# Performance work log

Hardware: AMD Instinct MI355X
Metric: run time of the kernel (lower is better)

The kernel has to match this reference:

```python
import jax, jax.numpy as jnp
import numpy as np

# S6Layer dims: d_model=256; internal d_state=max(8,16//2)=8; expand=max(1.5,2*0.75)=1.5 -> d_inner=384
B, L, DM = 8, 4096, 256
DI, DS = 384, 8
CHUNK = 32  # seq_len > 64 path: chunked scan, state resets to 0 at every chunk (faithful to source)
EPS = 1e-5


def setup_inputs() -> dict:
    key = jax.random.key(0)
    ks = jax.random.split(key, 8)
    def w(k, shape, s=0.02):
        return jax.random.normal(k, shape, jnp.float32) * s
    return {
        "x": jax.random.normal(ks[0], (B, L, DM), jnp.float32),
        "gamma": jnp.ones((DM,), jnp.float32),
        "beta": jnp.zeros((DM,), jnp.float32),
        "W_in": w(ks[1], (3 * DI, DM)),
        "b_in": jnp.zeros((3 * DI,), jnp.float32),
        "W_dt": w(ks[2], (DI, DI)),
        "b_dt": jnp.zeros((DI,), jnp.float32),
        "A_log": jax.random.normal(ks[3], (DI, DS), jnp.float32),
        "D_vec": jax.random.normal(ks[4], (DI,), jnp.float32),
        "W_out": w(ks[5], (DM, DI)),
        "b_out": jnp.zeros((DM,), jnp.float32),
    }


def _layernorm(x, g, b):
    mu = jnp.mean(x, axis=-1, keepdims=True)
    var = jnp.mean(jnp.square(x - mu), axis=-1, keepdims=True)
    return (x - mu) * jax.lax.rsqrt(var + EPS) * g + b


def _chunked_scan(xp, dt, A):
    # xp, dt: [B, L, DI]; A: [DI, DS]. Each CHUNK-length block scans from h=0
    # (the torch code never propagates h across chunks for seq_len > 64).
    C = L // CHUNK
    xr = xp.reshape(B, C, CHUNK, DI)
    dtr = dt.reshape(B, C, CHUNK, DI)
    dA = jnp.exp(dtr[..., None] * A)              # [B, C, T, DI, DS]
    dA_t = jnp.moveaxis(dA, 2, 0)                 # [T, B, C, DI, DS]
    x_t = jnp.moveaxis(xr, 2, 0)                  # [T, B, C, DI]

    def step(h, inp):
        dA_i, x_i = inp
        h = h * dA_i + x_i[..., None]             # broadcast x over DS
        return h, jnp.sum(h, axis=-1)             # y_i: [B, C, DI]

    h0 = jnp.zeros((B, C, DI, DS), xp.dtype)
    _, ys = jax.lax.scan(step, h0, (dA_t, x_t))   # ys: [T, B, C, DI]
    return jnp.moveaxis(ys, 0, 2).reshape(B, L, DI)


def reference(x, gamma, beta, W_in, b_in, W_dt, b_dt, A_log, D_vec, W_out, b_out):
    residual = x
    xn = _layernorm(x, gamma, beta)
    xz = xn @ W_in.T + b_in                       # [B, L, 3*DI]
    x_proj, z, dt_in = jnp.split(xz, 3, axis=-1)
    x_proj = jax.nn.silu(x_proj)
    z = jax.nn.silu(z)
    dt = jax.nn.softplus(dt_in @ W_dt.T + b_dt)   # [B, L, DI]
    A = -jnp.exp(A_log)                           # [DI, DS]
    y = _chunked_scan(x_proj, dt, A)
    y = y * z + x_proj * D_vec
    return y @ W_out.T + b_out + residual
```

## Files before the change

### kernel.cpp

```cpp
#include <hip/hip_runtime.h>
#include <stdint.h>

#define B_  8
#define L_  4096
#define DM  256
#define DI  384
#define DS  8
#define M_  (B_*L_)

typedef float f32x4 __attribute__((ext_vector_type(4)));
typedef short s16x8 __attribute__((ext_vector_type(8)));

#define AS1(p) ((__attribute__((address_space(1))) void*)(p))
#define AS3(p) ((__attribute__((address_space(3))) void*)(p))

__device__ __forceinline__ unsigned short f2bf(float f) {
  union { float f; uint32_t u; } v; v.f = f;
  uint32_t r = v.u + 0x7FFFu + ((v.u >> 16) & 1u);
  return (unsigned short)(r >> 16);
}
__device__ __forceinline__ float bf2f(unsigned short h) {
  union { uint32_t u; float f; } v; v.u = ((uint32_t)h) << 16;
  return v.f;
}
__device__ __forceinline__ float silu_f(float x) { return x / (1.f + __expf(-x)); }

__global__ __launch_bounds__(256) void cvt_kernel(
    const float* __restrict__ w0, const float* __restrict__ w1, const float* __restrict__ w2,
    unsigned short* __restrict__ o0, unsigned short* __restrict__ o1, unsigned short* __restrict__ o2) {
  int i = blockIdx.x * 256 + threadIdx.x;
  if (i < 3*DI*DM) o0[i] = f2bf(w0[i]);
  if (i < DI*DI)   o1[i] = f2bf(w1[i]);
  if (i < DM*DI)   o2[i] = f2bf(w2[i]);
}

__global__ __launch_bounds__(256) void ln_kernel(
    const float* __restrict__ x, const float* __restrict__ gamma, const float* __restrict__ beta,
    unsigned short* __restrict__ xn) {
  int token = blockIdx.x * 4 + (threadIdx.x >> 6);
  int lane  = threadIdx.x & 63;
  const float4 v = *(const float4*)(x + (size_t)token*DM + lane*4);
  float s  = v.x + v.y + v.z + v.w;
  float ss = v.x*v.x + v.y*v.y + v.z*v.z + v.w*v.w;
  #pragma unroll
  for (int off = 32; off > 0; off >>= 1) {
    s  += __shfl_xor(s,  off, 64);
    ss += __shfl_xor(ss, off, 64);
  }
  float mean = s * (1.f/DM);
  float var  = ss * (1.f/DM) - mean*mean;
  float rstd = rsqrtf(var + 1e-5f);
  const float4 g = *(const float4*)(gamma + lane*4);
  const float4 b = *(const float4*)(beta  + lane*4);
  ushort4 o;
  o.x = f2bf((v.x - mean)*rstd*g.x + b.x);
  o.y = f2bf((v.y - mean)*rstd*g.y + b.y);
  o.z = f2bf((v.z - mean)*rstd*g.z + b.z);
  o.w = f2bf((v.w - mean)*rstd*g.w + b.w);
  *(ushort4*)(xn + (size_t)token*DM + lane*4) = o;
}

template<int EPI, int CH>
__global__ __launch_bounds__(256, 2) void gemm_db(
    const unsigned short* __restrict__ A,
    const unsigned short* __restrict__ Bw,
    const float* __restrict__ bias,
    unsigned short* __restrict__ o_xp, unsigned short* __restrict__ o_z,
    unsigned short* __restrict__ o_dtin,
    unsigned short* __restrict__ o_bf,
    const float* __restrict__ resid, float* __restrict__ o_f)
{
  constexpr int K = CH * 64;
  __shared__ unsigned short smem[32768];

  const int t    = threadIdx.x;
  const int lane = t & 63;
  const int w    = t >> 6;
  const int wm   = (w & 1) * 64;
  const int wn   = (w >> 1) * 64;
  const int fr   = lane & 15;
  const int fq   = lane >> 4;
  const int mbase = blockIdx.x * 128;
  const int nbase = blockIdx.y * 128;

  const unsigned short* gA[4];
  const unsigned short* gB[4];
  int ldso[4];
  #pragma unroll
  for (int i = 0; i < 4; ++i) {
    int c   = i*256 + t;
    int row = c >> 3;
    int qs  = (c & 7) ^ (row & 7);
    gA[i] = A  + (size_t)(mbase + row)*K + qs*8;
    gB[i] = Bw + (size_t)(nbase + row)*K + qs*8;
    ldso[i] = c * 8;
  }

  auto issue = [&](int chunk) {
    const int buf = (chunk & 1) * 8192;
    #pragma unroll
    for (int i = 0; i < 4; ++i)
      __builtin_amdgcn_global_load_lds(AS1(gA[i] + chunk*64), AS3(smem + buf + ldso[i]), 16, 0, 0);
    #pragma unroll
    for (int i = 0; i < 4; ++i)
      __builtin_amdgcn_global_load_lds(AS1(gB[i] + chunk*64), AS3(smem + 16384 + buf + ldso[i]), 16, 0, 0);
  };

  f32x4 acc[4][4];
  #pragma unroll
  for (int mi = 0; mi < 4; ++mi)
    #pragma unroll
    for (int ni = 0; ni < 4; ++ni) acc[mi][ni] = (f32x4){0.f, 0.f, 0.f, 0.f};

  issue(0);
  __syncthreads();

  #pragma unroll
  for (int c = 0; c < CH; ++c) {
    if (c + 1 < CH) issue(c + 1);
    const unsigned short* sA = smem + (c & 1)*8192;
    const unsigned short* sB = smem + 16384 + (c & 1)*8192;
    #pragma unroll
    for (int h = 0; h < 2; ++h) {
      s16x8 af[4], bfr[4];
      #pragma unroll
      for (int mi = 0; mi < 4; ++mi) {
        int r  = wm + mi*16 + fr;
        int qs = (h*4 + fq) ^ (r & 7);
        af[mi] = *(const s16x8*)(sA + r*64 + qs*8);
      }
      #pragma unroll
      for (int ni = 0; ni < 4; ++ni) {
        int r  = wn + ni*16 + fr;
        int qs = (h*4 + fq) ^ (r & 7);
        bfr[ni] = *(const s16x8*)(sB + r*64 + qs*8);
      }
      #pragma unroll
      for (int mi = 0; mi < 4; ++mi)
        #pragma unroll
        for (int ni = 0; ni < 4; ++ni)
          acc[mi][ni] = __builtin_amdgcn_mfma_f32_16x16x32_bf16(af[mi], bfr[ni], acc[mi][ni], 0, 0, 0);
    }
    __syncthreads();
  }

  if constexpr (EPI == 3) {
    #pragma unroll
    for (int ni = 0; ni < 4; ++ni) {
      int gn = nbase + wn + ni*16 + fr;
      float bv = bias[gn];
      #pragma unroll
      for (int mi = 0; mi < 4; ++mi) {
        int gm0 = mbase + wm + mi*16 + fq*4;
        #pragma unroll
        for (int r = 0; r < 4; ++r) {
          size_t gm = (size_t)(gm0 + r);
          o_f[gm*DM + gn] = acc[mi][ni][r] + bv + resid[gm*DM + gn];
        }
      }
    }
  } else {
    const bool do_silu = (EPI == 1) && (blockIdx.y < 6);
    #pragma unroll
    for (int ni = 0; ni < 4; ++ni) {
      int cn = wn + ni*16 + fr;
      float bv = bias[nbase + cn];
      #pragma unroll
      for (int mi = 0; mi < 4; ++mi) {
        int rm0 = wm + mi*16 + fq*4;
        #pragma unroll
        for (int r = 0; r < 4; ++r) {
          float cval = acc[mi][ni][r] + bv;
          if constexpr (EPI == 1) { if (do_silu) cval = silu_f(cval); }
          else                    { cval = (cval > 20.f) ? cval : log1pf(__expf(cval)); }
          smem[(rm0 + r)*136 + cn] = f2bf(cval);
        }
      }
    }
    __syncthreads();
    unsigned short* dst;
    int colbase;
    if constexpr (EPI == 1) {
      int p = blockIdx.y;
      dst = (p < 3) ? o_xp : (p < 6) ? o_z : o_dtin;
      colbase = (p % 3) * 128;
    } else {
      dst = o_bf; colbase = nbase;
    }
    const int rr = t >> 4, cc = (t & 15) * 8;
    #pragma unroll
    for (int it = 0; it < 8; ++it) {
      int row = rr + it*16;
      s16x8 v = *(const s16x8*)(smem + row*136 + cc);
      *(s16x8*)(dst + (size_t)(mbase + row)*DI + colbase + cc) = v;
    }
  }
}

__global__ __launch_bounds__(384) void scan_kernel(
    const unsigned short* __restrict__ xp, const unsigned short* __restrict__ dt,
    const unsigned short* __restrict__ zb, const float* __restrict__ A_log,
    const float* __restrict__ D_vec, unsigned short* __restrict__ yz) {
  int g  = blockIdx.x;
  int di = threadIdx.x;
  size_t base = (size_t)g * 32 * DI + di;
  float a[DS];
  #pragma unroll
  for (int s = 0; s < DS; ++s) a[s] = -__expf(A_log[di*DS + s]);
  float Dv = D_vec[di];
  float h[DS] = {0.f,0.f,0.f,0.f,0.f,0.f,0.f,0.f};
  for (int tt = 0; tt < 32; ++tt) {
    size_t idx = base + (size_t)tt * DI;
    float xv  = bf2f(xp[idx]);
    float dtv = bf2f(dt[idx]);
    float y = 0.f;
    #pragma unroll
    for (int s = 0; s < DS; ++s) {
      h[s] = h[s] * __expf(dtv * a[s]) + xv;
      y += h[s];
    }
    float zv = bf2f(zb[idx]);
    yz[idx] = f2bf(y * zv + xv * Dv);
  }
}

extern "C" void kernel_launch(void* const* d_in, const int* in_sizes, int n_in,
                              void* d_out, int out_size, void* d_ws, size_t ws_size,
                              hipStream_t stream) {
  const float* x     = (const float*)d_in[0];
  const float* gamma = (const float*)d_in[1];
  const float* beta  = (const float*)d_in[2];
  const float* W_in  = (const float*)d_in[3];
  const float* b_in  = (const float*)d_in[4];
  const float* W_dt  = (const float*)d_in[5];
  const float* b_dt  = (const float*)d_in[6];
  const float* A_log = (const float*)d_in[7];
  const float* D_vec = (const float*)d_in[8];
  const float* W_out = (const float*)d_in[9];
  const float* b_out = (const float*)d_in[10];
  float* out = (float*)d_out;

  char* ws = (char*)d_ws;
  size_t off = 0;
  auto alloc = [&](size_t bytes) -> char* {
    char* p = ws + off; off += (bytes + 255) & ~(size_t)255; return p;
  };
  unsigned short* xn    = (unsigned short*)alloc((size_t)M_*DM*2);
  unsigned short* xpb   = (unsigned short*)alloc((size_t)M_*DI*2);
  unsigned short* zb    = (unsigned short*)alloc((size_t)M_*DI*2);
  unsigned short* dtin  = (unsigned short*)alloc((size_t)M_*DI*2);
  unsigned short* dtb   = (unsigned short*)alloc((size_t)M_*DI*2);
  unsigned short* yzb   = dtin;
  unsigned short* winb  = (unsigned short*)alloc((size_t)3*DI*DM*2);
  unsigned short* wdtb  = (unsigned short*)alloc((size_t)DI*DI*2);
  unsigned short* woutb = (unsigned short*)alloc((size_t)DM*DI*2);

  cvt_kernel<<<dim3((3*DI*DM + 255)/256), 256, 0, stream>>>(W_in, W_dt, W_out, winb, wdtb, woutb);
  ln_kernel<<<dim3(M_/4), 256, 0, stream>>>(x, gamma, beta, xn);
  gemm_db<1, 4><<<dim3(M_/128, (3*DI)/128), 256, 0, stream>>>(
      xn, winb, b_in, xpb, zb, dtin, nullptr, nullptr, nullptr);
  gemm_db<2, 6><<<dim3(M_/128, DI/128), 256, 0, stream>>>(
      dtin, wdtb, b_dt, nullptr, nullptr, nullptr, dtb, nullptr, nullptr);
  scan_kernel<<<dim3(M_/32), DI, 0, stream>>>(xpb, dtb, zb, A_log, D_vec, yzb);
  gemm_db<3, 6><<<dim3(M_/128, DM/128), 256, 0, stream>>>(
      yzb, woutb, b_out, nullptr, nullptr, nullptr, nullptr, x, out);
}
```

Before: 246.8 us.

## Hold GEMM weight fragments in registers and shrink M tile to 64

The GEMM kernel now loads each wave's full-K slice of the weight matrix straight from global memory into registers once, and stages only the activation tile through LDS. The M tile shrinks from 128 to 64 rows and each wave covers 32 output columns, which cuts LDS use and the number of LDS reads per MFMA. This is meant to remove LDS traffic and raise occupancy. In exchange it uses many more VGPRs (up to 24 fragments for K=384), repeats the weight load in every block, and has lower arithmetic intensity per block.

```diff
diff --git a/kernel.cpp b/kernel.cpp
--- a/kernel.cpp
+++ b/kernel.cpp
@@ -60,8 +60,8 @@
   *(ushort4*)(xn + (size_t)token*DM + lane*4) = o;
 }
 
-template<int EPI, int CH>
-__global__ __launch_bounds__(256, 2) void gemm_db(
+template<int EPI, int CH, int WPE>
+__global__ __launch_bounds__(256, WPE) void gemm_breg(
     const unsigned short* __restrict__ A,
     const unsigned short* __restrict__ Bw,
     const float* __restrict__ bias,
@@ -70,88 +70,83 @@
     unsigned short* __restrict__ o_bf,
     const float* __restrict__ resid, float* __restrict__ o_f)
 {
-  constexpr int K = CH * 64;
-  __shared__ unsigned short smem[32768];
+  constexpr int K  = CH * 64;
+  constexpr int KS = CH * 2;
+  __shared__ unsigned short smem[8704];
 
   const int t    = threadIdx.x;
   const int lane = t & 63;
   const int w    = t >> 6;
-  const int wm   = (w & 1) * 64;
-  const int wn   = (w >> 1) * 64;
+  const int wn   = w * 32;
   const int fr   = lane & 15;
   const int fq   = lane >> 4;
-  const int mbase = blockIdx.x * 128;
+  const int mbase = blockIdx.x * 64;
   const int nbase = blockIdx.y * 128;
 
-  const unsigned short* gA[4];
-  const unsigned short* gB[4];
-  int ldso[4];
-  #pragma unroll
-  for (int i = 0; i < 4; ++i) {
+  const unsigned short* gA[2];
+  int ldso[2];
+  #pragma unroll
+  for (int i = 0; i < 2; ++i) {
     int c   = i*256 + t;
     int row = c >> 3;
     int qs  = (c & 7) ^ (row & 7);
-    gA[i] = A  + (size_t)(mbase + row)*K + qs*8;
-    gB[i] = Bw + (size_t)(nbase + row)*K + qs*8;
+    gA[i]   = A + (size_t)(mbase + row)*K + qs*8;
     ldso[i] = c * 8;
   }
-
   auto issue = [&](int chunk) {
-    const int buf = (chunk & 1) * 8192;
-    #pragma unroll
-    for (int i = 0; i < 4; ++i)
+    const int buf = (chunk & 1) * 4096;
+    #pragma unroll
+    for (int i = 0; i < 2; ++i)
       __builtin_amdgcn_global_load_lds(AS1(gA[i] + chunk*64), AS3(smem + buf + ldso[i]), 16, 0, 0);
-    #pragma unroll
-    for (int i = 0; i < 4; ++i)
-      __builtin_amdgcn_global_load_lds(AS1(gB[i] + chunk*64), AS3(smem + 16384 + buf + ldso[i]), 16, 0, 0);
   };
 
-  f32x4 acc[4][4];
+  issue(0);
+
+  s16x8 breg[KS][2];
+  #pragma unroll
+  for (int ks = 0; ks < KS; ++ks)
+    #pragma unroll
+    for (int ni = 0; ni < 2; ++ni)
+      breg[ks][ni] = *(const s16x8*)(Bw + (size_t)(nbase + wn + ni*16 + fr)*K + ks*32 + fq*8);
+
+  f32x4 acc[4][2];
   #pragma unroll
   for (int mi = 0; mi < 4; ++mi)
     #pragma unroll
-    for (int ni = 0; ni < 4; ++ni) acc[mi][ni] = (f32x4){0.f, 0.f, 0.f, 0.f};
-
-  issue(0);
+    for (int ni = 0; ni < 2; ++ni) acc[mi][ni] = (f32x4){0.f, 0.f, 0.f, 0.f};
+
   __syncthreads();
 
   #pragma unroll
   for (int c = 0; c < CH; ++c) {
     if (c + 1 < CH) issue(c + 1);
-    const unsigned short* sA = smem + (c & 1)*8192;
-    const unsigned short* sB = smem + 16384 + (c & 1)*8192;
+    const unsigned short* sA = smem + (c & 1)*4096;
     #pragma unroll
     for (int h = 0; h < 2; ++h) {
-      s16x8 af[4], bfr[4];
+      s16x8 af[4];
       #pragma unroll
       for (int mi = 0; mi < 4; ++mi) {
-        int r  = wm + mi*16 + fr;
+        int r  = mi*16 + fr;
         int qs = (h*4 + fq) ^ (r & 7);
         af[mi] = *(const s16x8*)(sA + r*64 + qs*8);
       }
       #pragma unroll
-      for (int ni = 0; ni < 4; ++ni) {
-        int r  = wn + ni*16 + fr;
-        int qs = (h*4 + fq) ^ (r & 7);
-        bfr[ni] = *(const s16x8*)(sB + r*64 + qs*8);
-      }
-      #pragma unroll
       for (int mi = 0; mi < 4; ++mi)
         #pragma unroll
-        for (int ni = 0; ni < 4; ++ni)
-          acc[mi][ni] = __builtin_amdgcn_mfma_f32_16x16x32_bf16(af[mi], bfr[ni], acc[mi][ni], 0, 0, 0);
+        for (int ni = 0; ni < 2; ++ni)
+          acc[mi][ni] = __builtin_amdgcn_mfma_f32_16x16x32_bf16(af[mi], breg[c*2+h][ni], acc[mi][ni], 0, 0, 0);
     }
     __syncthreads();
   }
 
   if constexpr (EPI == 3) {
     #pragma unroll
-    for (int ni = 0; ni < 4; ++ni) {
+    for (int ni = 0; ni < 2; ++ni) {
       int gn = nbase + wn + ni*16 + fr;
       float bv = bias[gn];
       #pragma unroll
       for (int mi = 0; mi < 4; ++mi) {
-        int gm0 = mbase + wm + mi*16 + fq*4;
+        int gm0 = mbase + mi*16 + fq*4;
         #pragma unroll
         for (int r = 0; r < 4; ++r) {
           size_t gm = (size_t)(gm0 + r);
@@ -162,12 +157,12 @@
   } else {
     const bool do_silu = (EPI == 1) && (blockIdx.y < 6);
     #pragma unroll
-    for (int ni = 0; ni < 4; ++ni) {
+    for (int ni = 0; ni < 2; ++ni) {
       int cn = wn + ni*16 + fr;
       float bv = bias[nbase + cn];
       #pragma unroll
       for (int mi = 0; mi < 4; ++mi) {
-        int rm0 = wm + mi*16 + fq*4;
+        int rm0 = mi*16 + fq*4;
         #pragma unroll
         for (int r = 0; r < 4; ++r) {
           float cval = acc[mi][ni][r] + bv;
@@ -189,7 +184,7 @@
     }
     const int rr = t >> 4, cc = (t & 15) * 8;
     #pragma unroll
-    for (int it = 0; it < 8; ++it) {
+    for (int it = 0; it < 4; ++it) {
       int row = rr + it*16;
       s16x8 v = *(const s16x8*)(smem + row*136 + cc);
       *(s16x8*)(dst + (size_t)(mbase + row)*DI + colbase + cc) = v;
@@ -257,11 +252,11 @@
 
   cvt_kernel<<<dim3((3*DI*DM + 255)/256), 256, 0, stream>>>(W_in, W_dt, W_out, winb, wdtb, woutb);
   ln_kernel<<<dim3(M_/4), 256, 0, stream>>>(x, gamma, beta, xn);
-  gemm_db<1, 4><<<dim3(M_/128, (3*DI)/128), 256, 0, stream>>>(
+  gemm_breg<1, 4, 3><<<dim3(M_/64, 9), 256, 0, stream>>>(
       xn, winb, b_in, xpb, zb, dtin, nullptr, nullptr, nullptr);
-  gemm_db<2, 6><<<dim3(M_/128, DI/128), 256, 0, stream>>>(
+  gemm_breg<2, 6, 2><<<dim3(M_/64, 3), 256, 0, stream>>>(
       dtin, wdtb, b_dt, nullptr, nullptr, nullptr, dtb, nullptr, nullptr);
   scan_kernel<<<dim3(M_/32), DI, 0, stream>>>(xpb, dtb, zb, A_log, D_vec, yzb);
-  gemm_db<3, 6><<<dim3(M_/128, DM/128), 256, 0, stream>>>(
+  gemm_breg<3, 6, 2><<<dim3(M_/64, 2), 256, 0, stream>>>(
       yzb, woutb, b_out, nullptr, nullptr, nullptr, nullptr, x, out);
 }
```

Result: slower. 254.5 us (+3.1%).

## Halve GEMM K-chunk and use k-major LDS layout to fit four blocks per CU

Applied to the files above, without the earlier changes.

Cuts the GEMM K-step from 64 to 32 and shrinks shared memory from 64KB to about 34KB per block, raising the launch-bounds occupancy hint from 2 to 4 blocks per CU. The LDS tile is reorganised from a swizzled row-major layout to a k-quad-major layout (q*1024 + row*8), so each MFMA fragment read is a contiguous 16-byte slot without XOR swizzle. The goal is better latency hiding through more resident waves, at the cost of twice as many loop iterations and barriers per tile. It also risks register spilling under the tighter bound and LDS bank conflicts from the new layout.

```diff
diff --git a/kernel.cpp b/kernel.cpp
--- a/kernel.cpp
+++ b/kernel.cpp
@@ -61,7 +61,7 @@
 }
 
 template<int EPI, int CH>
-__global__ __launch_bounds__(256, 2) void gemm_db(
+__global__ __launch_bounds__(256, 4) void gemm_l4(
     const unsigned short* __restrict__ A,
     const unsigned short* __restrict__ Bw,
     const float* __restrict__ bias,
@@ -70,8 +70,8 @@
     unsigned short* __restrict__ o_bf,
     const float* __restrict__ resid, float* __restrict__ o_f)
 {
-  constexpr int K = CH * 64;
-  __shared__ unsigned short smem[32768];
+  constexpr int K = CH * 32;
+  __shared__ unsigned short smem[17408];
 
   const int t    = threadIdx.x;
   const int lane = t & 63;
@@ -83,27 +83,26 @@
   const int mbase = blockIdx.x * 128;
   const int nbase = blockIdx.y * 128;
 
-  const unsigned short* gA[4];
-  const unsigned short* gB[4];
-  int ldso[4];
-  #pragma unroll
-  for (int i = 0; i < 4; ++i) {
+  const unsigned short* gA[2];
+  const unsigned short* gB[2];
+  int ldso[2];
+  #pragma unroll
+  for (int i = 0; i < 2; ++i) {
     int c   = i*256 + t;
-    int row = c >> 3;
-    int qs  = (c & 7) ^ (row & 7);
-    gA[i] = A  + (size_t)(mbase + row)*K + qs*8;
-    gB[i] = Bw + (size_t)(nbase + row)*K + qs*8;
+    int q   = c >> 7;
+    int row = c & 127;
+    gA[i] = A  + (size_t)(mbase + row)*K + q*8;
+    gB[i] = Bw + (size_t)(nbase + row)*K + q*8;
     ldso[i] = c * 8;
   }
-
   auto issue = [&](int chunk) {
-    const int buf = (chunk & 1) * 8192;
-    #pragma unroll
-    for (int i = 0; i < 4; ++i)
-      __builtin_amdgcn_global_load_lds(AS1(gA[i] + chunk*64), AS3(smem + buf + ldso[i]), 16, 0, 0);
-    #pragma unroll
-    for (int i = 0; i < 4; ++i)
-      __builtin_amdgcn_global_load_lds(AS1(gB[i] + chunk*64), AS3(smem + 16384 + buf + ldso[i]), 16, 0, 0);
+    const int buf = (chunk & 1) * 4096;
+    #pragma unroll
+    for (int i = 0; i < 2; ++i)
+      __builtin_amdgcn_global_load_lds(AS1(gA[i] + chunk*32), AS3(smem + buf + ldso[i]), 16, 0, 0);
+    #pragma unroll
+    for (int i = 0; i < 2; ++i)
+      __builtin_amdgcn_global_load_lds(AS1(gB[i] + chunk*32), AS3(smem + 8192 + buf + ldso[i]), 16, 0, 0);
   };
 
   f32x4 acc[4][4];
@@ -118,29 +117,20 @@
   #pragma unroll
   for (int c = 0; c < CH; ++c) {
     if (c + 1 < CH) issue(c + 1);
-    const unsigned short* sA = smem + (c & 1)*8192;
-    const unsigned short* sB = smem + 16384 + (c & 1)*8192;
-    #pragma unroll
-    for (int h = 0; h < 2; ++h) {
-      s16x8 af[4], bfr[4];
+    const unsigned short* sA = smem + (c & 1)*4096;
+    const unsigned short* sB = smem + 8192 + (c & 1)*4096;
+    s16x8 af[4], bfr[4];
+    #pragma unroll
+    for (int mi = 0; mi < 4; ++mi)
+      af[mi] = *(const s16x8*)(sA + fq*1024 + (wm + mi*16 + fr)*8);
+    #pragma unroll
+    for (int ni = 0; ni < 4; ++ni)
+      bfr[ni] = *(const s16x8*)(sB + fq*1024 + (wn + ni*16 + fr)*8);
+    #pragma unroll
+    for (int mi = 0; mi < 4; ++mi)
       #pragma unroll
-      for (int mi = 0; mi < 4; ++mi) {
-        int r  = wm + mi*16 + fr;
-        int qs = (h*4 + fq) ^ (r & 7);
-        af[mi] = *(const s16x8*)(sA + r*64 + qs*8);
-      }
-      #pragma unroll
-      for (int ni = 0; ni < 4; ++ni) {
-        int r  = wn + ni*16 + fr;
-        int qs = (h*4 + fq) ^ (r & 7);
-        bfr[ni] = *(const s16x8*)(sB + r*64 + qs*8);
-      }
-      #pragma unroll
-      for (int mi = 0; mi < 4; ++mi)
-        #pragma unroll
-        for (int ni = 0; ni < 4; ++ni)
-          acc[mi][ni] = __builtin_amdgcn_mfma_f32_16x16x32_bf16(af[mi], bfr[ni], acc[mi][ni], 0, 0, 0);
-    }
+      for (int ni = 0; ni < 4; ++ni)
+        acc[mi][ni] = __builtin_amdgcn_mfma_f32_16x16x32_bf16(af[mi], bfr[ni], acc[mi][ni], 0, 0, 0);
     __syncthreads();
   }
 
@@ -257,11 +247,11 @@
 
   cvt_kernel<<<dim3((3*DI*DM + 255)/256), 256, 0, stream>>>(W_in, W_dt, W_out, winb, wdtb, woutb);
   ln_kernel<<<dim3(M_/4), 256, 0, stream>>>(x, gamma, beta, xn);
-  gemm_db<1, 4><<<dim3(M_/128, (3*DI)/128), 256, 0, stream>>>(
+  gemm_l4<1, 8><<<dim3(M_/128, 9), 256, 0, stream>>>(
       xn, winb, b_in, xpb, zb, dtin, nullptr, nullptr, nullptr);
-  gemm_db<2, 6><<<dim3(M_/128, DI/128), 256, 0, stream>>>(
+  gemm_l4<2, 12><<<dim3(M_/128, 3), 256, 0, stream>>>(
       dtin, wdtb, b_dt, nullptr, nullptr, nullptr, dtb, nullptr, nullptr);
   scan_kernel<<<dim3(M_/32), DI, 0, stream>>>(xpb, dtb, zb, A_log, D_vec, yzb);
-  gemm_db<3, 6><<<dim3(M_/128, DM/128), 256, 0, stream>>>(
+  gemm_l4<3, 12><<<dim3(M_/128, 2), 256, 0, stream>>>(
       yzb, woutb, b_out, nullptr, nullptr, nullptr, nullptr, x, out);
 }
```

Result: slower. 263.7 us (+6.9%).
